# Performance work log

Hardware: AMD Instinct MI355X
Metric: run time of the kernel (lower is better)

Reference implementation:

```python
import jax, jax.numpy as jnp
import numpy as np
from jax import lax

B, CIN, L = 2, 768, 1024
DM, DI, DS, DTR, DC = 512, 1024, 16, 32, 4  # d_model, d_inner, d_state, dt_rank, d_conv


def _conv1d(x, w, b, pad, groups=1):
    # x: (B, Cin, L), w: (Cout, Cin//groups, K)
    y = lax.conv_general_dilated(x, w, (1,), [pad], dimension_numbers=('NCH', 'OIH', 'NCH'),
                                 feature_group_count=groups)
    return y + b[None, :, None]


def _gnorm(x, g, b, groups=32, eps=1e-5):
    Bx, C, Lx = x.shape
    xg = x.reshape(Bx, groups, C // groups, Lx)
    m = xg.mean((2, 3), keepdims=True)
    v = xg.var((2, 3), keepdims=True)
    xg = (xg - m) * lax.rsqrt(v + eps)
    return xg.reshape(Bx, C, Lx) * g[None, :, None] + b[None, :, None]


def _selective_scan(u, delta, A, Bm, Cm, D):
    # u, delta: (B, L, DI); Bm, Cm: (B, L, DS); A: (DI, DS); D: (DI,)
    def step(h, inp):
        d, b, c, x = inp  # d,x: (B,DI); b,c: (B,DS)
        h = jnp.exp(d[..., None] * A) * h + (d * x)[..., None] * b[:, None, :]
        y = jnp.einsum('bds,bs->bd', h, c)
        return h, y
    h0 = jnp.zeros((u.shape[0], A.shape[0], A.shape[1]), u.dtype)
    xs = tuple(jnp.moveaxis(t, 1, 0) for t in (delta, Bm, Cm, u))
    _, ys = lax.scan(step, h0, xs)
    return jnp.moveaxis(ys, 0, 1) + u * D


def _mamba_dir(xz, cv_w, cv_b, xp_w, dt_w, dt_b, Alog, D):
    x, z = jnp.split(xz, 2, axis=1)                       # each (B, DI, L)
    x = _conv1d(x, cv_w, cv_b, (DC - 1, 0), groups=DI)    # causal depthwise conv
    x = jax.nn.silu(x)
    xT = x.transpose(0, 2, 1)                             # (B, L, DI)
    x_dbl = xT @ xp_w.T                                   # (B, L, DTR+2*DS)
    dt, Bm, Cm = jnp.split(x_dbl, [DTR, DTR + DS], axis=-1)
    delta = jax.nn.softplus(dt @ dt_w.T + dt_b)           # (B, L, DI)
    y = _selective_scan(xT, delta, -jnp.exp(Alog), Bm, Cm, D)
    return y * jax.nn.silu(z.transpose(0, 2, 1))


def _forward(x, conv1_w, conv1_b, gn1_g, gn1_b, conv2_w, conv2_b, gn2_g, gn2_b,
             conv3_w, conv3_b, gn3_g, gn3_b, ln_g, ln_b, in_proj_w, out_proj_w,
             cv_w_f, cv_b_f, xp_w_f, dt_w_f, dt_b_f, Alog_f, D_f,
             cv_w_r, cv_b_r, xp_w_r, dt_w_r, dt_b_r, Alog_r, D_r):
    # CNN stem: (Conv1d k3 p1 -> GroupNorm(32) -> ReLU) x 3, 768->128->256->512
    h = jax.nn.relu(_gnorm(_conv1d(x, conv1_w, conv1_b, (1, 1)), gn1_g, gn1_b))
    h = jax.nn.relu(_gnorm(_conv1d(h, conv2_w, conv2_b, (1, 1)), gn2_g, gn2_b))
    h = jax.nn.relu(_gnorm(_conv1d(h, conv3_w, conv3_b, (1, 1)), gn3_g, gn3_b))  # (B,512,L)
    res = h
    # MaskMambaBlock: LayerNorm -> bidirectional ViM -> residual; mask is all-ones (no-op)
    t = h.transpose(0, 2, 1)                               # (B, L, DM)
    mu = t.mean(-1, keepdims=True)
    var = t.var(-1, keepdims=True)
    t = (t - mu) * lax.rsqrt(var + 1e-5) * ln_g + ln_b
    xz = (t @ in_proj_w.T).transpose(0, 2, 1)              # (B, 2*DI, L) shared for both dirs
    yf = _mamba_dir(xz, cv_w_f, cv_b_f, xp_w_f, dt_w_f, dt_b_f, Alog_f, D_f)
    yr = _mamba_dir(jnp.flip(xz, -1), cv_w_r, cv_b_r, xp_w_r, dt_w_r, dt_b_r, Alog_r, D_r)
    y = yf + jnp.flip(yr, 1)                               # (B, L, DI)
    out = (y @ out_proj_w.T).transpose(0, 2, 1)            # (B, DM, L)
    return res + out


def setup_inputs() -> dict:
    key = jax.random.key(0)
    ks = iter(jax.random.split(key, 64))
    p = lambda shape, s=0.02: jax.random.normal(next(ks), shape, jnp.float32) * s
    d = {"x": jax.random.normal(next(ks), (B, CIN, L), jnp.float32)}
    for i, (ci, co) in enumerate([(CIN, 128), (128, 256), (256, 512)], 1):
        d[f"conv{i}_w"] = p((co, ci, 3))
        d[f"conv{i}_b"] = jnp.zeros((co,))
        d[f"gn{i}_g"] = jnp.ones((co,))
        d[f"gn{i}_b"] = jnp.zeros((co,))
    d["ln_g"] = jnp.ones((DM,))
    d["ln_b"] = jnp.zeros((DM,))
    d["in_proj_w"] = p((2 * DI, DM))
    d["out_proj_w"] = p((DM, DI))
    for s in ("f", "r"):
        d[f"cv_w_{s}"] = p((DI, 1, DC), 0.1)
        d[f"cv_b_{s}"] = jnp.zeros((DI,))
        d[f"xp_w_{s}"] = p((DTR + 2 * DS, DI))
        d[f"dt_w_{s}"] = p((DI, DTR), 0.1)
        d[f"dt_b_{s}"] = p((DI,), 0.5) - 4.0  # softplus(dt) small, like Mamba dt init
        d[f"Alog_{s}"] = jnp.log(jnp.tile(jnp.arange(1, DS + 1, dtype=jnp.float32)[None, :], (DI, 1)))
        d[f"D_{s}"] = jnp.ones((DI,))
    return d


def reference(x, conv1_w, conv1_b, gn1_g, gn1_b, conv2_w, conv2_b, gn2_g, gn2_b,
              conv3_w, conv3_b, gn3_g, gn3_b, ln_g, ln_b, in_proj_w, out_proj_w,
              cv_w_f, cv_b_f, xp_w_f, dt_w_f, dt_b_f, Alog_f, D_f,
              cv_w_r, cv_b_r, xp_w_r, dt_w_r, dt_b_r, Alog_r, D_r):
    return _forward(x, conv1_w, conv1_b, gn1_g, gn1_b, conv2_w, conv2_b, gn2_g, gn2_b,
                    conv3_w, conv3_b, gn3_g, gn3_b, ln_g, ln_b, in_proj_w, out_proj_w,
                    cv_w_f, cv_b_f, xp_w_f, dt_w_f, dt_b_f, Alog_f, D_f,
                    cv_w_r, cv_b_r, xp_w_r, dt_w_r, dt_b_r, Alog_r, D_r)
```

## Files before the change

kernel.cpp:

```cpp
#include <hip/hip_runtime.h>
#include <hip/hip_bf16.h>
#include <math.h>

#define LL 1024
#define NC 16
#define CS 64

typedef __attribute__((ext_vector_type(8))) short short8_t;
typedef __attribute__((ext_vector_type(4))) float f32x4;

__device__ __forceinline__ float sigmoidf_(float x){ return 1.f/(1.f+__expf(-x)); }
__device__ __forceinline__ unsigned short f2bu(float x){
  unsigned int u = __float_as_uint(x);
  unsigned int r = (u + 0x7fffu + ((u>>16)&1u)) >> 16;
  return (unsigned short)r;
}
__device__ __forceinline__ float bu2f(unsigned short u){
  return __uint_as_float(((unsigned int)u)<<16);
}

__global__ __launch_bounds__(256) void gn_relu_k(
    float* __restrict__ io, const float* __restrict__ g, const float* __restrict__ bt,
    int C, int Cg)
{
  int b = blockIdx.x >> 5;
  int grp = blockIdx.x & 31;
  int n = Cg * LL;
  float* p = io + ((size_t)b*C + (size_t)grp*Cg)*LL;
  int tid = threadIdx.x;
  float s=0.f, s2=0.f;
  for (int i=tid; i<n; i+=256){ float v=p[i]; s+=v; s2+=v*v; }
  __shared__ float red[10];
  #pragma unroll
  for (int off=32; off; off>>=1){ s+=__shfl_down(s,off); s2+=__shfl_down(s2,off); }
  if ((tid&63)==0){ red[tid>>6]=s; red[4+(tid>>6)]=s2; }
  __syncthreads();
  if (tid==0){
    float S=red[0]+red[1]+red[2]+red[3];
    float S2=red[4]+red[5]+red[6]+red[7];
    float mean = S/(float)n;
    float var = S2/(float)n - mean*mean;
    red[8]=mean; red[9]=rsqrtf(var+1e-5f);
  }
  __syncthreads();
  float mean=red[8], rstd=red[9];
  const float* gp = g + grp*Cg;
  const float* bp = bt + grp*Cg;
  for (int i=tid; i<n; i+=256){
    int co = i >> 10;
    float v = (p[i]-mean)*rstd*gp[co] + bp[co];
    p[i] = fmaxf(v, 0.f);
  }
}

__global__ __launch_bounds__(64) void ln_k(
    const float* __restrict__ h, const float* __restrict__ g, const float* __restrict__ bt,
    float* __restrict__ tout)
{
  int bl = blockIdx.x;
  int b = bl >> 10, l = bl & 1023;
  int lane = threadIdx.x;
  const float* base = h + (size_t)b*512*LL + l;
  float v[8]; float s=0.f, s2=0.f;
  #pragma unroll
  for (int j=0;j<8;++j){ v[j] = base[(size_t)(lane + j*64)*LL]; s+=v[j]; s2+=v[j]*v[j]; }
  #pragma unroll
  for (int off=32; off; off>>=1){ s+=__shfl_xor(s,off); s2+=__shfl_xor(s2,off); }
  float mean = s*(1.f/512.f);
  float rstd = rsqrtf(s2*(1.f/512.f) - mean*mean + 1e-5f);
  float* o = tout + (size_t)bl*512;
  #pragma unroll
  for (int j=0;j<8;++j){ int c = lane + j*64; o[c] = (v[j]-mean)*rstd*g[c] + bt[c]; }
}

template<int MODE>
__global__ __launch_bounds__(256) void reduceK_k(
    const float* __restrict__ P, const float* __restrict__ bias,
    const float* __restrict__ res, float* __restrict__ out,
    int M, int N, int KS)
{
  int i = blockIdx.x*256 + threadIdx.x;
  if (i >= N*M) return;
  float s = 0.f;
  for (int k=0;k<KS;++k) s += P[(size_t)k*((size_t)N*M) + i];
  if (MODE==0){ out[i] = s; return; }
  int n = i / M, m = i - n*M;
  int b = n >> 10, l = n & 1023;
  size_t o = ((size_t)b*M + m)*LL + l;
  if (MODE==1) out[o] = s + bias[m];
  else         out[o] = s + res[o];
}

__global__ __launch_bounds__(256) void ts_split3_k(
    const float* __restrict__ src, unsigned short* __restrict__ dst, int Cin)
{
  __shared__ float sx[32][35];
  int b = blockIdx.z;
  int l0 = blockIdx.x*32, ci0 = blockIdx.y*32;
  int tid = threadIdx.x;
  const float* sb = src + ((size_t)b*Cin + ci0)*LL;
  for (int idx = tid; idx < 32*34; idx += 256){
    int r = idx / 34, c = idx - r*34;
    int lp = l0 - 1 + c;
    sx[r][c] = (lp >= 0 && lp < LL) ? sb[(size_t)r*LL + lp] : 0.f;
  }
  __syncthreads();
  int K = 3*Cin, K3 = 9*Cin;
  int lr = tid >> 5, cl = tid & 31;
  #pragma unroll
  for (int p=0;p<4;++p){
    int l = lr + p*8;
    unsigned short* drow = dst + (size_t)(b*LL + l0 + l)*K3;
    #pragma unroll
    for (int tap=0; tap<3; ++tap){
      float v = sx[cl][l + tap];
      unsigned short hi = f2bu(v);
      unsigned short lo = f2bu(v - bu2f(hi));
      int kk = tap*Cin + ci0 + cl;
      drow[kk] = hi; drow[K + kk] = hi; drow[2*K + kk] = lo;
    }
  }
}

__global__ __launch_bounds__(256) void wsplit3_conv_k(
    const float* __restrict__ w, unsigned short* __restrict__ dst, int Cout, int Cin)
{
  int i = blockIdx.x*256 + threadIdx.x;
  if (i >= Cout*Cin) return;
  int co = i / Cin, ci = i - co*Cin;
  int K = 3*Cin, K3 = 9*Cin;
  unsigned short* drow = dst + (size_t)co*K3;
  #pragma unroll
  for (int tap=0; tap<3; ++tap){
    float v = w[(size_t)(co*Cin + ci)*3 + tap];
    unsigned short hi = f2bu(v);
    unsigned short lo = f2bu(v - bu2f(hi));
    int kk = tap*Cin + ci;
    drow[kk] = hi; drow[K + kk] = lo; drow[2*K + kk] = hi;
  }
}

template<int PAT>
__global__ __launch_bounds__(256) void split3_k(
    const float* __restrict__ src, unsigned short* __restrict__ dst,
    int R, int K, int ld)
{
  int i = blockIdx.x*256 + threadIdx.x;
  int kq = K >> 2;
  if (i >= R*kq) return;
  int r = i / kq, k4 = (i - r*kq)*4;
  float4 v = *(const float4*)&src[(size_t)r*ld + k4];
  float vv[4] = {v.x, v.y, v.z, v.w};
  unsigned short hi[4], lo[4];
  #pragma unroll
  for (int j=0;j<4;++j){ hi[j]=f2bu(vv[j]); lo[j]=f2bu(vv[j]-bu2f(hi[j])); }
  unsigned short* d0 = dst + (size_t)r*3*K + k4;
  ushort4 h4 = make_ushort4(hi[0],hi[1],hi[2],hi[3]);
  ushort4 l4 = make_ushort4(lo[0],lo[1],lo[2],lo[3]);
  *(ushort4*)d0 = h4;
  *(ushort4*)(d0 + K)   = (PAT==0) ? l4 : h4;
  *(ushort4*)(d0 + 2*K) = (PAT==0) ? h4 : l4;
}

__global__ __launch_bounds__(256) void split1_k(
    const float* __restrict__ src, unsigned short* __restrict__ dst,
    int R, int K, int ld, int k0)
{
  int i = blockIdx.x*256 + threadIdx.x;
  int kq = K >> 2;
  if (i >= R*kq) return;
  int r = i / kq, k4 = (i - r*kq)*4;
  float4 v = *(const float4*)&src[(size_t)r*ld + k0 + k4];
  *(ushort4*)(dst + (size_t)r*K + k4) =
      make_ushort4(f2bu(v.x), f2bu(v.y), f2bu(v.z), f2bu(v.w));
}

__global__ __launch_bounds__(256) void gated_split_k(
    const float* __restrict__ y0, const float* __restrict__ y1,
    const float* __restrict__ xz, unsigned short* __restrict__ dst)
{
  __shared__ float sz[32][33];
  int b = blockIdx.z;
  int l0 = blockIdx.x*32, d0 = blockIdx.y*32;
  int tid = threadIdx.x;
  const float* zb = xz + ((size_t)b*2048 + 1024 + d0)*LL + l0;
  for (int idx = tid; idx < 1024; idx += 256){
    int r = idx >> 5, c = idx & 31;
    sz[r][c] = zb[(size_t)r*LL + c];
  }
  __syncthreads();
  int lr = tid >> 5, dd = tid & 31;
  #pragma unroll
  for (int p=0;p<4;++p){
    int l = lr + p*8;
    size_t n = (size_t)b*LL + l0 + l;
    float zv = sz[dd][l];
    float y = y0[n*1024 + d0 + dd] + y1[n*1024 + d0 + dd];
    dst[n*1024 + d0 + dd] = f2bu(y * (zv * sigmoidf_(zv)));
  }
}

template<int BM, int EPI>
__global__ __launch_bounds__(256) void gemm_bf3(
    const unsigned short* __restrict__ A, const unsigned short* __restrict__ B,
    const float* __restrict__ bias, void* __restrict__ Cv,
    int M, int N, int K3)
{
  constexpr int BN = 64;
  constexpr int AIT = (BM*4)/256;
  constexpr int FM = BM/32;
  __shared__ __align__(16) char smem[(BM+BN)*80];
  char* As = smem;
  char* Bs = smem + BM*80;
  int tid = threadIdx.x;
  int n0 = blockIdx.x*BN, m0 = blockIdx.y*BM;
  int kper = K3 / gridDim.z;
  int kbeg = blockIdx.z * kper;
  int w = tid >> 6, lane = tid & 63;
  int wm = w & 1, wn = w >> 1;
  f32x4 acc[FM][2];
  #pragma unroll
  for (int i=0;i<FM;++i){ acc[i][0] = (f32x4){0,0,0,0}; acc[i][1] = (f32x4){0,0,0,0}; }

  uint4 areg[AIT]; uint4 breg;
  auto load_stage = [&](int k){
    #pragma unroll
    for (int i=0;i<AIT;++i){
      int idx = tid + i*256;
      areg[i] = *(const uint4*)&A[(size_t)(m0 + (idx>>2))*K3 + k + (idx&3)*8];
    }
    breg = *(const uint4*)&B[(size_t)(n0 + (tid>>2))*K3 + k + (tid&3)*8];
  };
  load_stage(kbeg);
  for (int k = kbeg; k < kbeg + kper; k += 32){
    __syncthreads();
    #pragma unroll
    for (int i=0;i<AIT;++i){
      int idx = tid + i*256;
      *(uint4*)&As[(idx>>2)*80 + (idx&3)*16] = areg[i];
    }
    *(uint4*)&Bs[(tid>>2)*80 + (tid&3)*16] = breg;
    __syncthreads();
    if (k + 32 < kbeg + kper) load_stage(k + 32);
    int g16 = (lane>>4)*16, r16 = lane&15;
    short8_t bf0 = *(short8_t*)&Bs[(wn*32 + r16)*80 + g16];
    short8_t bf1 = *(short8_t*)&Bs[(wn*32 + 16 + r16)*80 + g16];
    #pragma unroll
    for (int i2=0;i2<FM;++i2){
      short8_t af = *(short8_t*)&As[(wm*(BM/2) + i2*16 + r16)*80 + g16];
      acc[i2][0] = __builtin_amdgcn_mfma_f32_16x16x32_bf16(af, bf0, acc[i2][0], 0,0,0);
      acc[i2][1] = __builtin_amdgcn_mfma_f32_16x16x32_bf16(af, bf1, acc[i2][1], 0,0,0);
    }
  }
  #pragma unroll
  for (int i2=0;i2<FM;++i2){
    #pragma unroll
    for (int j=0;j<2;++j){
      #pragma unroll
      for (int r=0;r<4;++r){
        int m = m0 + wm*(BM/2) + i2*16 + ((lane>>4)*4 + r);
        int n = n0 + wn*32 + j*16 + (lane&15);
        float v = acc[i2][j][r];
        if (EPI==0){
          ((float*)Cv)[(size_t)blockIdx.z*((size_t)N*M) + (size_t)n*M + m] = v;
        } else if (EPI==1){
          int b = n>>10, l = n&1023;
          ((float*)Cv)[((size_t)b*M + m)*LL + l] = v;
        } else {
          float xv = v + bias[m];
          float sp = (xv > 20.f) ? xv : log1pf(__expf(xv));
          ((unsigned short*)Cv)[(size_t)n*M + m] = f2bu(sp);
        }
      }
    }
  }
}

__global__ __launch_bounds__(256) void dwconv_k(
    const float* __restrict__ xz, const float* __restrict__ cw,
    const float* __restrict__ cb, unsigned short* __restrict__ outT, int rev)
{
  __shared__ float sx[64][73];
  int l0 = blockIdx.x * 64;
  int d0 = blockIdx.y * 64;
  int b = blockIdx.z;
  int tid = threadIdx.x;
  const float* base = xz + ((size_t)b*2048 + d0)*LL;
  for (int idx = tid; idx < 64*67; idx += 256) {
    int r = idx / 67, i = idx - r*67;
    int lp = l0 - 3 + i;
    float v = 0.f;
    if (lp >= 0) v = base[(size_t)r*LL + (rev ? (LL-1-lp) : lp)];
    sx[r][i] = v;
  }
  __syncthreads();
  int dof = tid & 63;
  int lq = tid >> 6;
  int d = d0 + dof;
  float4 w4 = *(const float4*)(cw + (size_t)d*4);
  float bv = cb[d];
  unsigned short* orow = outT + (size_t)b*LL*1024 + d;
  #pragma unroll
  for (int j=0;j<16;++j){
    int lr = lq + j*4;
    float acc = bv + w4.x*sx[dof][lr] + w4.y*sx[dof][lr+1]
                   + w4.z*sx[dof][lr+2] + w4.w*sx[dof][lr+3];
    orow[(size_t)(l0+lr)*1024] = f2bu(acc * sigmoidf_(acc));
  }
}

__global__ __launch_bounds__(256) void scan1_k(
    const unsigned short* __restrict__ de0, const unsigned short* __restrict__ de1,
    const unsigned short* __restrict__ u0, const unsigned short* __restrict__ u1,
    const float* __restrict__ xd0, const float* __restrict__ xd1,
    const float* __restrict__ al0, const float* __restrict__ al1,
    float* __restrict__ Pbuf, float* __restrict__ Sbuf)
{
  __shared__ float sBC[CS][32];
  int zc = blockIdx.z, dir = zc>>1, b = zc&1;
  const unsigned short* de = dir? de1:de0;
  const unsigned short* uT = dir? u1:u0;
  const float* xd = dir? xd1:xd0;
  const float* al = dir? al1:al0;
  int t = threadIdx.x;
  int d = blockIdx.x*128 + (t>>1);
  int sh = (t&1)*8;
  int l0 = blockIdx.y*CS;
  size_t nrow = (size_t)b*1024 + l0;
  for (int idx = t; idx < CS*32; idx += 256){
    int r = idx >> 5, c = idx & 31;
    sBC[r][c] = xd[(nrow + r)*64 + 32 + c];
  }
  __syncthreads();
  float A[8], h[8], P[8];
  #pragma unroll
  for (int j=0;j<8;++j){ A[j] = -expf(al[d*16 + sh + j]); h[j]=0.f; P[j]=1.f; }
  const unsigned short* dep = de + nrow*1024 + d;
  const unsigned short* up  = uT + nrow*1024 + d;
  for (int l=0; l<CS; ++l){
    float dv = bu2f(dep[(size_t)l*1024]);
    float uv = bu2f(up[(size_t)l*1024]);
    float du = dv*uv;
    #pragma unroll
    for (int j=0;j<8;++j){
      float a = __expf(dv*A[j]);
      h[j] = a*h[j] + du*sBC[l][sh+j];
      P[j] *= a;
    }
  }
  size_t sb = (size_t)blockIdx.y*65536 + (size_t)(zc*1024 + d)*16 + sh;
  *(float4*)&Pbuf[sb]   = make_float4(P[0],P[1],P[2],P[3]);
  *(float4*)&Pbuf[sb+4] = make_float4(P[4],P[5],P[6],P[7]);
  *(float4*)&Sbuf[sb]   = make_float4(h[0],h[1],h[2],h[3]);
  *(float4*)&Sbuf[sb+4] = make_float4(h[4],h[5],h[6],h[7]);
}

__global__ __launch_bounds__(256) void scan2_k(
    const float* __restrict__ Pbuf, const float* __restrict__ Sbuf,
    float* __restrict__ Hbuf)
{
  int seq = blockIdx.x*256 + threadIdx.x;
  float H = 0.f;
  #pragma unroll
  for (int cch=0; cch<NC; ++cch){
    Hbuf[(size_t)cch*65536 + seq] = H;
    H = Pbuf[(size_t)cch*65536 + seq]*H + Sbuf[(size_t)cch*65536 + seq];
  }
}

__global__ __launch_bounds__(256) void scan3_k(
    const unsigned short* __restrict__ de0, const unsigned short* __restrict__ de1,
    const unsigned short* __restrict__ u0, const unsigned short* __restrict__ u1,
    const float* __restrict__ xd0, const float* __restrict__ xd1,
    const float* __restrict__ al0, const float* __restrict__ al1,
    const float* __restrict__ dd0, const float* __restrict__ dd1,
    const float* __restrict__ Hbuf,
    float* __restrict__ y0, float* __restrict__ y1)
{
  __shared__ float sBC[CS][32];
  int zc = blockIdx.z, dir = zc>>1, b = zc&1;
  const unsigned short* de = dir? de1:de0;
  const unsigned short* uT = dir? u1:u0;
  const float* xd = dir? xd1:xd0;
  const float* al = dir? al1:al0;
  const float* DD = dir? dd1:dd0;
  float* y = dir? y1:y0;
  int t = threadIdx.x;
  int d = blockIdx.x*128 + (t>>1);
  int sh = (t&1)*8;
  int l0 = blockIdx.y*CS;
  size_t nrow = (size_t)b*1024 + l0;
  for (int idx = t; idx < CS*32; idx += 256){
    int r = idx >> 5, c = idx & 31;
    sBC[r][c] = xd[(nrow + r)*64 + 32 + c];
  }
  __syncthreads();
  float A[8], h[8];
  size_t sb = (size_t)blockIdx.y*65536 + (size_t)(zc*1024 + d)*16 + sh;
  float4 h03 = *(const float4*)&Hbuf[sb];
  float4 h47 = *(const float4*)&Hbuf[sb+4];
  h[0]=h03.x; h[1]=h03.y; h[2]=h03.z; h[3]=h03.w;
  h[4]=h47.x; h[5]=h47.y; h[6]=h47.z; h[7]=h47.w;
  #pragma unroll
  for (int j=0;j<8;++j) A[j] = -expf(al[d*16 + sh + j]);
  float Dd = DD[d];
  const unsigned short* dep = de + nrow*1024 + d;
  const unsigned short* up  = uT + nrow*1024 + d;
  float* yb = y + (size_t)b*LL*1024 + d;
  for (int l=0; l<CS; ++l){
    float dv = bu2f(dep[(size_t)l*1024]);
    float uv = bu2f(up[(size_t)l*1024]);
    float du = dv*uv;
    float pa = 0.f;
    #pragma unroll
    for (int j=0;j<8;++j){
      float a = __expf(dv*A[j]);
      h[j] = a*h[j] + du*sBC[l][sh+j];
      pa += h[j]*sBC[l][16+sh+j];
    }
    pa += __shfl_xor(pa, 1);
    if ((t&1)==0){
      int lo = dir ? (1023 - l0 - l) : (l0 + l);
      yb[(size_t)lo*1024] = pa + uv*Dd;
    }
  }
}

extern "C" void kernel_launch(void* const* d_in, const int* in_sizes, int n_in,
                              void* d_out, int out_size, void* d_ws, size_t ws_size,
                              hipStream_t stream)
{
  const float* x   = (const float*)d_in[0];
  const float* c1w = (const float*)d_in[1];  const float* c1b = (const float*)d_in[2];
  const float* g1g = (const float*)d_in[3];  const float* g1b = (const float*)d_in[4];
  const float* c2w = (const float*)d_in[5];  const float* c2b = (const float*)d_in[6];
  const float* g2g = (const float*)d_in[7];  const float* g2b = (const float*)d_in[8];
  const float* c3w = (const float*)d_in[9];  const float* c3b = (const float*)d_in[10];
  const float* g3g = (const float*)d_in[11]; const float* g3b = (const float*)d_in[12];
  const float* lng = (const float*)d_in[13]; const float* lnb = (const float*)d_in[14];
  const float* ipw = (const float*)d_in[15]; const float* opw = (const float*)d_in[16];
  const float* cvw[2]  = {(const float*)d_in[17], (const float*)d_in[24]};
  const float* cvb[2]  = {(const float*)d_in[18], (const float*)d_in[25]};
  const float* xpw[2]  = {(const float*)d_in[19], (const float*)d_in[26]};
  const float* dtw[2]  = {(const float*)d_in[20], (const float*)d_in[27]};
  const float* dtb[2]  = {(const float*)d_in[21], (const float*)d_in[28]};
  const float* alog[2] = {(const float*)d_in[22], (const float*)d_in[29]};
  const float* Dp[2]   = {(const float*)d_in[23], (const float*)d_in[30]};

  float* ws = (float*)d_ws;
  float* h3  = ws;
  float* h1  = ws + 1048576;
  float* h2  = ws + 1310720;
  float* t   = ws + 1835008;
  float* xzb = ws + 2883584;
  unsigned short* Wb = (unsigned short*)(ws + 7077888);
  unsigned short* Bsb = (unsigned short*)(ws + 8650752);
  float* yy0 = ws + 11796480;
  float* yy1 = ws + 13893632;
  float* PART = ws + 15990784;
  unsigned short* xcv[2] = { (unsigned short*)(ws + 18087936),
                             (unsigned short*)(ws + 18087936) + 2097152 };
  float* xdb[2] = { ws + 1048576, ws + 1179648 };
  unsigned short* dl[2] = { (unsigned short*)PART, (unsigned short*)PART + 2097152 };
  float* Pb = ws + 2883584;
  float* Sb = ws + 4980736;
  float* Hb = ws + 1835008;
  float* pxp = ws + 8650752;
  unsigned short* dtB = (unsigned short*)(ws + 9175040);
  float* out = (float*)d_out;

  ts_split3_k<<<dim3(32,24,2), 256, 0, stream>>>(x, Bsb, 768);
  wsplit3_conv_k<<<384, 256, 0, stream>>>(c1w, Wb, 128, 768);
  gemm_bf3<128,0><<<dim3(32,1,8), 256, 0, stream>>>(Wb, Bsb, nullptr, PART, 128, 2048, 6912);
  reduceK_k<1><<<1024, 256, 0, stream>>>(PART, c1b, nullptr, h1, 128, 2048, 8);
  gn_relu_k<<<64, 256, 0, stream>>>(h1, g1g, g1b, 128, 4);

  ts_split3_k<<<dim3(32,4,2), 256, 0, stream>>>(h1, Bsb, 128);
  wsplit3_conv_k<<<128, 256, 0, stream>>>(c2w, Wb, 256, 128);
  gemm_bf3<128,0><<<dim3(32,2,4), 256, 0, stream>>>(Wb, Bsb, nullptr, PART, 256, 2048, 1152);
  reduceK_k<1><<<2048, 256, 0, stream>>>(PART, c2b, nullptr, h2, 256, 2048, 4);
  gn_relu_k<<<64, 256, 0, stream>>>(h2, g2g, g2b, 256, 8);

  ts_split3_k<<<dim3(32,8,2), 256, 0, stream>>>(h2, Bsb, 256);
  wsplit3_conv_k<<<512, 256, 0, stream>>>(c3w, Wb, 512, 256);
  gemm_bf3<128,0><<<dim3(32,4,2), 256, 0, stream>>>(Wb, Bsb, nullptr, PART, 512, 2048, 2304);
  reduceK_k<1><<<4096, 256, 0, stream>>>(PART, c3b, nullptr, h3, 512, 2048, 2);
  gn_relu_k<<<64, 256, 0, stream>>>(h3, g3g, g3b, 512, 16);

  ln_k<<<2048, 64, 0, stream>>>(h3, lng, lnb, t);
  split3_k<0><<<1024, 256, 0, stream>>>(ipw, Wb, 2048, 512, 512);
  split3_k<1><<<1024, 256, 0, stream>>>(t, Bsb, 2048, 512, 512);
  gemm_bf3<128,1><<<dim3(32,16,1), 256, 0, stream>>>(Wb, Bsb, nullptr, xzb, 2048, 2048, 1536);

  dwconv_k<<<dim3(16,16,2), 256, 0, stream>>>(xzb, cvw[0], cvb[0], xcv[0], 0);
  dwconv_k<<<dim3(16,16,2), 256, 0, stream>>>(xzb, cvw[1], cvb[1], xcv[1], 1);
  for (int s2=0; s2<2; ++s2){
    split1_k<<<64, 256, 0, stream>>>(xpw[s2], Wb, 64, 1024, 1024, 0);
    gemm_bf3<64,0><<<dim3(32,1,4), 256, 0, stream>>>(Wb, xcv[s2], nullptr, pxp, 64, 2048, 1024);
    reduceK_k<0><<<512, 256, 0, stream>>>(pxp, nullptr, nullptr, xdb[s2], 64, 2048, 4);
    split1_k<<<32, 256, 0, stream>>>(dtw[s2], Wb, 1024, 32, 32, 0);
    split1_k<<<64, 256, 0, stream>>>(xdb[s2], dtB, 2048, 32, 64, 0);
    gemm_bf3<128,2><<<dim3(32,8,1), 256, 0, stream>>>(Wb, dtB, dtb[s2], dl[s2], 1024, 2048, 32);
  }

  scan1_k<<<dim3(8,NC,4), 256, 0, stream>>>(
      dl[0], dl[1], xcv[0], xcv[1], xdb[0], xdb[1], alog[0], alog[1], Pb, Sb);
  scan2_k<<<256, 256, 0, stream>>>(Pb, Sb, Hb);
  scan3_k<<<dim3(8,NC,4), 256, 0, stream>>>(
      dl[0], dl[1], xcv[0], xcv[1], xdb[0], xdb[1], alog[0], alog[1],
      Dp[0], Dp[1], Hb, yy0, yy1);

  gated_split_k<<<dim3(32,32,2), 256, 0, stream>>>(yy0, yy1, xzb, Bsb);
  split1_k<<<512, 256, 0, stream>>>(opw, Wb, 512, 1024, 1024, 0);
  gemm_bf3<128,0><<<dim3(32,4,2), 256, 0, stream>>>(Wb, Bsb, nullptr, PART, 512, 2048, 1024);
  reduceK_k<2><<<4096, 256, 0, stream>>>(PART, nullptr, h3, out, 512, 2048, 2);
}
```

Measured before the change: 542.2 us.

## Load GEMM tiles directly to LDS with XOR swizzle and wider K tiles

The bf16 MFMA GEMM now uses global_load_lds to copy A/B tiles straight into shared memory, with an XOR-swizzled layout and a K tile of 64 (or 32). This replaces the register-staged prefetch with padded rows. Several launches are retuned to smaller BM and fewer K-splits, and the x_proj reduce now also writes the bf16 dt slice, which removes one split kernel. The trade-off is that global-load latency is no longer overlapped with compute, since the register double-buffering is gone.

```diff
diff --git a/kernel.cpp b/kernel.cpp
--- a/kernel.cpp
+++ b/kernel.cpp
@@ -17,6 +17,11 @@
 }
 __device__ __forceinline__ float bu2f(unsigned short u){
   return __uint_as_float(((unsigned int)u)<<16);
+}
+__device__ __forceinline__ void gl2lds16(const void* g, void* l){
+  __builtin_amdgcn_global_load_lds(
+      (const __attribute__((address_space(1))) unsigned int*)g,
+      (__attribute__((address_space(3))) unsigned int*)l, 16, 0, 0);
 }
 
 __global__ __launch_bounds__(256) void gn_relu_k(
@@ -77,13 +82,19 @@
 __global__ __launch_bounds__(256) void reduceK_k(
     const float* __restrict__ P, const float* __restrict__ bias,
     const float* __restrict__ res, float* __restrict__ out,
-    int M, int N, int KS)
+    int M, int N, int KS, unsigned short* __restrict__ d16)
 {
   int i = blockIdx.x*256 + threadIdx.x;
   if (i >= N*M) return;
   float s = 0.f;
   for (int k=0;k<KS;++k) s += P[(size_t)k*((size_t)N*M) + i];
   if (MODE==0){ out[i] = s; return; }
+  if (MODE==3){
+    out[i] = s;
+    int c = i & 63;
+    if (c < 32) d16[(size_t)(i>>6)*32 + c] = f2bu(s);
+    return;
+  }
   int n = i / M, m = i - n*M;
   int b = n >> 10, l = n & 1023;
   size_t o = ((size_t)b*M + m)*LL + l;
@@ -200,57 +211,68 @@
   }
 }
 
-template<int BM, int EPI>
+template<int BM, int BK, int EPI>
 __global__ __launch_bounds__(256) void gemm_bf3(
     const unsigned short* __restrict__ A, const unsigned short* __restrict__ B,
     const float* __restrict__ bias, void* __restrict__ Cv,
     int M, int N, int K3)
 {
   constexpr int BN = 64;
-  constexpr int AIT = (BM*4)/256;
+  constexpr int RB = 2*BK;
+  constexpr int RPL = 1024/RB;
+  constexpr int ALD = BM/RPL;
+  constexpr int BLD = BN/RPL;
+  constexpr int NL = ALD + BLD;
   constexpr int FM = BM/32;
-  __shared__ __align__(16) char smem[(BM+BN)*80];
+  constexpr int KH = BK/32;
+  __shared__ __align__(16) char smem[(BM+BN)*RB];
   char* As = smem;
-  char* Bs = smem + BM*80;
+  char* Bs = smem + BM*RB;
   int tid = threadIdx.x;
+  int w = tid >> 6, lane = tid & 63;
+  int wm = w & 1, wn = w >> 1;
   int n0 = blockIdx.x*BN, m0 = blockIdx.y*BM;
   int kper = K3 / gridDim.z;
   int kbeg = blockIdx.z * kper;
-  int w = tid >> 6, lane = tid & 63;
-  int wm = w & 1, wn = w >> 1;
+
+  int lr, sc;
+  if (BK == 64){ lr = lane>>3; sc = (lane&7) ^ lr; }
+  else         { lr = lane>>2; sc = (lane&3) ^ ((lr>>1)&3); }
+  size_t lsrc = (size_t)lr*K3 + sc*8;
+
   f32x4 acc[FM][2];
   #pragma unroll
   for (int i=0;i<FM;++i){ acc[i][0] = (f32x4){0,0,0,0}; acc[i][1] = (f32x4){0,0,0,0}; }
 
-  uint4 areg[AIT]; uint4 breg;
-  auto load_stage = [&](int k){
-    #pragma unroll
-    for (int i=0;i<AIT;++i){
-      int idx = tid + i*256;
-      areg[i] = *(const uint4*)&A[(size_t)(m0 + (idx>>2))*K3 + k + (idx&3)*8];
-    }
-    breg = *(const uint4*)&B[(size_t)(n0 + (tid>>2))*K3 + k + (tid&3)*8];
-  };
-  load_stage(kbeg);
-  for (int k = kbeg; k < kbeg + kper; k += 32){
+  int r16 = lane & 15, g4 = lane >> 4;
+  for (int k = kbeg; k < kbeg + kper; k += BK){
+    for (int j = w; j < NL; j += 4){
+      if (j < ALD){
+        gl2lds16(A + (size_t)(m0 + j*RPL)*K3 + k + lsrc, As + j*(RPL*RB));
+      } else {
+        int jb = j - ALD;
+        gl2lds16(B + (size_t)(n0 + jb*RPL)*K3 + k + lsrc, Bs + jb*(RPL*RB));
+      }
+    }
     __syncthreads();
     #pragma unroll
-    for (int i=0;i<AIT;++i){
-      int idx = tid + i*256;
-      *(uint4*)&As[(idx>>2)*80 + (idx&3)*16] = areg[i];
-    }
-    *(uint4*)&Bs[(tid>>2)*80 + (tid&3)*16] = breg;
+    for (int kh=0; kh<KH; ++kh){
+      int c = kh*4 + g4;
+      int rb0 = wn*32 + r16, rb1 = rb0 + 16;
+      int pb0 = (BK==64) ? (c ^ (rb0&7)) : (c ^ ((rb0>>1)&3));
+      int pb1 = (BK==64) ? (c ^ (rb1&7)) : (c ^ ((rb1>>1)&3));
+      short8_t bf0 = *(short8_t*)&Bs[rb0*RB + pb0*16];
+      short8_t bf1 = *(short8_t*)&Bs[rb1*RB + pb1*16];
+      #pragma unroll
+      for (int i2=0;i2<FM;++i2){
+        int ra = wm*(BM/2) + i2*16 + r16;
+        int pa = (BK==64) ? (c ^ (ra&7)) : (c ^ ((ra>>1)&3));
+        short8_t af = *(short8_t*)&As[ra*RB + pa*16];
+        acc[i2][0] = __builtin_amdgcn_mfma_f32_16x16x32_bf16(af, bf0, acc[i2][0], 0,0,0);
+        acc[i2][1] = __builtin_amdgcn_mfma_f32_16x16x32_bf16(af, bf1, acc[i2][1], 0,0,0);
+      }
+    }
     __syncthreads();
-    if (k + 32 < kbeg + kper) load_stage(k + 32);
-    int g16 = (lane>>4)*16, r16 = lane&15;
-    short8_t bf0 = *(short8_t*)&Bs[(wn*32 + r16)*80 + g16];
-    short8_t bf1 = *(short8_t*)&Bs[(wn*32 + 16 + r16)*80 + g16];
-    #pragma unroll
-    for (int i2=0;i2<FM;++i2){
-      short8_t af = *(short8_t*)&As[(wm*(BM/2) + i2*16 + r16)*80 + g16];
-      acc[i2][0] = __builtin_amdgcn_mfma_f32_16x16x32_bf16(af, bf0, acc[i2][0], 0,0,0);
-      acc[i2][1] = __builtin_amdgcn_mfma_f32_16x16x32_bf16(af, bf1, acc[i2][1], 0,0,0);
-    }
   }
   #pragma unroll
   for (int i2=0;i2<FM;++i2){
@@ -258,8 +280,8 @@
     for (int j=0;j<2;++j){
       #pragma unroll
       for (int r=0;r<4;++r){
-        int m = m0 + wm*(BM/2) + i2*16 + ((lane>>4)*4 + r);
-        int n = n0 + wn*32 + j*16 + (lane&15);
+        int m = m0 + wm*(BM/2) + i2*16 + (g4*4 + r);
+        int n = n0 + wn*32 + j*16 + r16;
         float v = acc[i2][j][r];
         if (EPI==0){
           ((float*)Cv)[(size_t)blockIdx.z*((size_t)N*M) + (size_t)n*M + m] = v;
@@ -471,36 +493,35 @@
 
   ts_split3_k<<<dim3(32,24,2), 256, 0, stream>>>(x, Bsb, 768);
   wsplit3_conv_k<<<384, 256, 0, stream>>>(c1w, Wb, 128, 768);
-  gemm_bf3<128,0><<<dim3(32,1,8), 256, 0, stream>>>(Wb, Bsb, nullptr, PART, 128, 2048, 6912);
-  reduceK_k<1><<<1024, 256, 0, stream>>>(PART, c1b, nullptr, h1, 128, 2048, 8);
+  gemm_bf3<64,64,0><<<dim3(32,2,4), 256, 0, stream>>>(Wb, Bsb, nullptr, PART, 128, 2048, 6912);
+  reduceK_k<1><<<1024, 256, 0, stream>>>(PART, c1b, nullptr, h1, 128, 2048, 4, nullptr);
   gn_relu_k<<<64, 256, 0, stream>>>(h1, g1g, g1b, 128, 4);
 
   ts_split3_k<<<dim3(32,4,2), 256, 0, stream>>>(h1, Bsb, 128);
   wsplit3_conv_k<<<128, 256, 0, stream>>>(c2w, Wb, 256, 128);
-  gemm_bf3<128,0><<<dim3(32,2,4), 256, 0, stream>>>(Wb, Bsb, nullptr, PART, 256, 2048, 1152);
-  reduceK_k<1><<<2048, 256, 0, stream>>>(PART, c2b, nullptr, h2, 256, 2048, 4);
+  gemm_bf3<64,64,0><<<dim3(32,4,2), 256, 0, stream>>>(Wb, Bsb, nullptr, PART, 256, 2048, 1152);
+  reduceK_k<1><<<2048, 256, 0, stream>>>(PART, c2b, nullptr, h2, 256, 2048, 2, nullptr);
   gn_relu_k<<<64, 256, 0, stream>>>(h2, g2g, g2b, 256, 8);
 
   ts_split3_k<<<dim3(32,8,2), 256, 0, stream>>>(h2, Bsb, 256);
   wsplit3_conv_k<<<512, 256, 0, stream>>>(c3w, Wb, 512, 256);
-  gemm_bf3<128,0><<<dim3(32,4,2), 256, 0, stream>>>(Wb, Bsb, nullptr, PART, 512, 2048, 2304);
-  reduceK_k<1><<<4096, 256, 0, stream>>>(PART, c3b, nullptr, h3, 512, 2048, 2);
+  gemm_bf3<128,64,0><<<dim3(32,4,2), 256, 0, stream>>>(Wb, Bsb, nullptr, PART, 512, 2048, 2304);
+  reduceK_k<1><<<4096, 256, 0, stream>>>(PART, c3b, nullptr, h3, 512, 2048, 2, nullptr);
   gn_relu_k<<<64, 256, 0, stream>>>(h3, g3g, g3b, 512, 16);
 
   ln_k<<<2048, 64, 0, stream>>>(h3, lng, lnb, t);
   split3_k<0><<<1024, 256, 0, stream>>>(ipw, Wb, 2048, 512, 512);
   split3_k<1><<<1024, 256, 0, stream>>>(t, Bsb, 2048, 512, 512);
-  gemm_bf3<128,1><<<dim3(32,16,1), 256, 0, stream>>>(Wb, Bsb, nullptr, xzb, 2048, 2048, 1536);
+  gemm_bf3<128,64,1><<<dim3(32,16,1), 256, 0, stream>>>(Wb, Bsb, nullptr, xzb, 2048, 2048, 1536);
 
   dwconv_k<<<dim3(16,16,2), 256, 0, stream>>>(xzb, cvw[0], cvb[0], xcv[0], 0);
   dwconv_k<<<dim3(16,16,2), 256, 0, stream>>>(xzb, cvw[1], cvb[1], xcv[1], 1);
   for (int s2=0; s2<2; ++s2){
     split1_k<<<64, 256, 0, stream>>>(xpw[s2], Wb, 64, 1024, 1024, 0);
-    gemm_bf3<64,0><<<dim3(32,1,4), 256, 0, stream>>>(Wb, xcv[s2], nullptr, pxp, 64, 2048, 1024);
-    reduceK_k<0><<<512, 256, 0, stream>>>(pxp, nullptr, nullptr, xdb[s2], 64, 2048, 4);
+    gemm_bf3<64,64,0><<<dim3(32,1,4), 256, 0, stream>>>(Wb, xcv[s2], nullptr, pxp, 64, 2048, 1024);
+    reduceK_k<3><<<512, 256, 0, stream>>>(pxp, nullptr, nullptr, xdb[s2], 64, 2048, 4, dtB);
     split1_k<<<32, 256, 0, stream>>>(dtw[s2], Wb, 1024, 32, 32, 0);
-    split1_k<<<64, 256, 0, stream>>>(xdb[s2], dtB, 2048, 32, 64, 0);
-    gemm_bf3<128,2><<<dim3(32,8,1), 256, 0, stream>>>(Wb, dtB, dtb[s2], dl[s2], 1024, 2048, 32);
+    gemm_bf3<128,32,2><<<dim3(32,8,1), 256, 0, stream>>>(Wb, dtB, dtb[s2], dl[s2], 1024, 2048, 32);
   }
 
   scan1_k<<<dim3(8,NC,4), 256, 0, stream>>>(
@@ -512,6 +533,6 @@
 
   gated_split_k<<<dim3(32,32,2), 256, 0, stream>>>(yy0, yy1, xzb, Bsb);
   split1_k<<<512, 256, 0, stream>>>(opw, Wb, 512, 1024, 1024, 0);
-  gemm_bf3<128,0><<<dim3(32,4,2), 256, 0, stream>>>(Wb, Bsb, nullptr, PART, 512, 2048, 1024);
-  reduceK_k<2><<<4096, 256, 0, stream>>>(PART, nullptr, h3, out, 512, 2048, 2);
-}
+  gemm_bf3<128,64,0><<<dim3(32,4,2), 256, 0, stream>>>(Wb, Bsb, nullptr, PART, 512, 2048, 1024);
+  reduceK_k<2><<<4096, 256, 0, stream>>>(PART, nullptr, h3, out, 512, 2048, 2, nullptr);
+}
```

Measured after the change: 492.5 us. 9.2% less time.
